# Optimization experiments

Hardware: AMD Instinct MI355X
Metric: run time of the kernel (lower is better)

## Reference

```python
import jax, jax.numpy as jnp
import numpy as np


def setup_inputs() -> dict:
    key = jax.random.key(0)
    k1, k2 = jax.random.split(key)
    n, B = 64, 256
    return {
        "out_matrix": jax.random.normal(k1, (n, n, B), dtype=jnp.float32),
        "label_matrix": jax.random.normal(k2, (n, n, B), dtype=jnp.float32),
        "margin": jnp.ones((), dtype=jnp.float32),
        "sample_num": 64,
    }


def reference(out_matrix, label_matrix, margin, sample_num):
    # out_matrix, label_matrix: [n, n, B]; sample_num == n (rows fully used).
    out = jnp.transpose(out_matrix, (2, 0, 1))   # [B, n, n]
    lab = jnp.transpose(label_matrix, (2, 0, 1))  # [B, n, n]
    # Per batch slice, per row r: pairwise diffs d[j,k] = out[r,j]-out[r,k]
    d = out[..., :, None] - out[..., None, :]     # [B, n, n, n]
    l = lab[..., :, None] - lab[..., None, :]     # [B, n, n, n]
    # Hinge: relu(margin - d*l), summed over everything (diagonal contributes margin,
    # matching the original which includes j==k terms).
    loss = jnp.sum(jax.nn.relu(margin - d * l))
    # flat_accuracy per batch slice: argmax over dim 1 of the [n,n] slice,
    # i.e. axis=2 of the [B,n,n] layout (torch argmax(preds,1) on squeezed slice).
    correction_num = jnp.sum(jnp.argmax(out, axis=2) == jnp.argmax(lab, axis=2))
    return loss, correction_num
```

## Files before the change

### kernel.cpp

```cpp
#include <hip/hip_runtime.h>
#include <math.h>


constexpr int N = 64;
constexpr int B = 256;
constexpr int BCHUNK = 64;
constexpr int NJG = 16;
constexpr int JI = 4;
constexpr int THREADS = BCHUNK * NJG;
constexpr int NBLK = N * (B / BCHUNK);

__global__ __launch_bounds__(THREADS)
void pm_hinge_partial(const float* __restrict__ outm,
                      const float* __restrict__ labm,
                      const float* __restrict__ margin,
                      float* __restrict__ ws)
{
    __shared__ float o_s[N * BCHUNK];
    __shared__ float l_s[N * BCHUNK];
    __shared__ float wsum[NJG];

    const int r   = blockIdx.x;
    const int b0  = blockIdx.y * BCHUNK;
    const int t   = threadIdx.x;
    const int blk = blockIdx.y * N + r;

    const float* src_o = outm + (size_t)r * (N * B) + b0;
    const float* src_l = labm + (size_t)r * (N * B) + b0;
#pragma unroll
    for (int f = t; f < (N * BCHUNK) / 4; f += THREADS) {
        const int j  = f >> 4;
        const int b4 = (f & 15) * 4;
        *(float4*)(&o_s[j * BCHUNK + b4]) = *(const float4*)(src_o + j * B + b4);
        *(float4*)(&l_s[j * BCHUNK + b4]) = *(const float4*)(src_l + j * B + b4);
    }
    __syncthreads();

    const float m  = margin[0];
    const int   b  = t & 63;
    const int   jg = t >> 6;

    float oj[JI], lj[JI];
#pragma unroll
    for (int i = 0; i < JI; ++i) {
        oj[i] = o_s[(jg + NJG * i) * BCHUNK + b];
        lj[i] = l_s[(jg + NJG * i) * BCHUNK + b];
    }

    float acc = 0.0f;

#define TERM(i) acc += fmaxf(fmaf(-(oj[i] - ok), lj[i] - lk, m), 0.0f)

#pragma unroll 4
    for (int k = jg + 1; k <= jg + 16; ++k) {
        const float ok = o_s[k * BCHUNK + b], lk = l_s[k * BCHUNK + b];
        TERM(0);
    }
#pragma unroll 4
    for (int k = jg + 17; k <= jg + 32; ++k) {
        const float ok = o_s[k * BCHUNK + b], lk = l_s[k * BCHUNK + b];
        TERM(0); TERM(1);
    }
#pragma unroll 4
    for (int k = jg + 33; k <= jg + 48; ++k) {
        const float ok = o_s[k * BCHUNK + b], lk = l_s[k * BCHUNK + b];
        TERM(0); TERM(1); TERM(2);
    }
#pragma unroll 2
    for (int k = jg + 49; k < N; ++k) {
        const float ok = o_s[k * BCHUNK + b], lk = l_s[k * BCHUNK + b];
        TERM(0); TERM(1); TERM(2); TERM(3);
    }
#undef TERM

    float cnt = 0.0f;
    if (t < 64) {
        const int bb = t;
        float bo = o_s[bb]; int io = 0;
        float bl = l_s[bb]; int il = 0;
#pragma unroll 4
        for (int j = 1; j < N; ++j) {
            const float vo = o_s[j * BCHUNK + bb];
            if (vo > bo) { bo = vo; io = j; }
            const float vl = l_s[j * BCHUNK + bb];
            if (vl > bl) { bl = vl; il = j; }
        }
        const unsigned long long mask = __ballot(io == il);
        cnt = (float)__popcll(mask);
    }

#pragma unroll
    for (int off = 32; off > 0; off >>= 1)
        acc += __shfl_down(acc, off, 64);
    if (b == 0) wsum[jg] = acc;
    __syncthreads();
    if (t == 0) {
        float s = 0.0f;
#pragma unroll
        for (int w = 0; w < NJG; ++w) s += wsum[w];
        ws[blk] = s;
        ws[NBLK + blk] = cnt;
    }
}

__global__ __launch_bounds__(64)
void pm_hinge_reduce(const float* __restrict__ ws,
                     const float* __restrict__ margin,
                     float* __restrict__ dout)
{
    const int t = threadIdx.x;
    float s = 0.0f, c = 0.0f;
#pragma unroll
    for (int i = 0; i < NBLK / 64; ++i) {
        s += ws[t + 64 * i];
        c += ws[NBLK + t + 64 * i];
    }
#pragma unroll
    for (int off = 32; off > 0; off >>= 1) {
        s += __shfl_down(s, off, 64);
        c += __shfl_down(c, off, 64);
    }
    if (t == 0) {
        const float m = margin[0];
        dout[0] = 2.0f * s + (float)(N * (size_t)N * B) * fmaxf(m, 0.0f);
        dout[1] = c;
    }
}

extern "C" void kernel_launch(void* const* d_in, const int* in_sizes, int n_in,
                              void* d_out, int out_size, void* d_ws, size_t ws_size,
                              hipStream_t stream) {
    const float* outm   = (const float*)d_in[0];
    const float* labm   = (const float*)d_in[1];
    const float* margin = (const float*)d_in[2];
    float* out = (float*)d_out;
    float* ws  = (float*)d_ws;

    pm_hinge_partial<<<dim3(N, B / BCHUNK), THREADS, 0, stream>>>(outm, labm, margin, ws);
    pm_hinge_reduce<<<1, 64, 0, stream>>>(ws, margin, out);
}
```

Baseline: 68.66 us.

## Interleave out/label in shared memory and widen per-thread j register blocking

Shared memory now stores out and label values interleaved as float2, so each k step needs a single 64-bit LDS load instead of two 32-bit loads. The thread count per block is halved (8 j-groups of 8 rows each), so every loaded k value is reused across up to 8 register-held j values and LDS traffic per pair term drops. The triangular loop is fully unrolled in 8-wide bands. In exchange each block has fewer waves to hide latency, register pressure rises, and the fully unrolled body grows larger.

```diff
diff --git a/kernel.cpp b/kernel.cpp
--- a/kernel.cpp
+++ b/kernel.cpp
@@ -5,8 +5,8 @@
 constexpr int N = 64;
 constexpr int B = 256;
 constexpr int BCHUNK = 64;
-constexpr int NJG = 16;
-constexpr int JI = 4;
+constexpr int NJG = 8;
+constexpr int JG = 8;
 constexpr int THREADS = BCHUNK * NJG;
 constexpr int NBLK = N * (B / BCHUNK);
 
@@ -16,8 +16,7 @@
                       const float* __restrict__ margin,
                       float* __restrict__ ws)
 {
-    __shared__ float o_s[N * BCHUNK];
-    __shared__ float l_s[N * BCHUNK];
+    __shared__ float2 ol[N * BCHUNK];
     __shared__ float wsum[NJG];
 
     const int r   = blockIdx.x;
@@ -31,59 +30,56 @@
     for (int f = t; f < (N * BCHUNK) / 4; f += THREADS) {
         const int j  = f >> 4;
         const int b4 = (f & 15) * 4;
-        *(float4*)(&o_s[j * BCHUNK + b4]) = *(const float4*)(src_o + j * B + b4);
-        *(float4*)(&l_s[j * BCHUNK + b4]) = *(const float4*)(src_l + j * B + b4);
+        const float4 vo = *(const float4*)(src_o + j * B + b4);
+        const float4 vl = *(const float4*)(src_l + j * B + b4);
+        float4 p0 = make_float4(vo.x, vl.x, vo.y, vl.y);
+        float4 p1 = make_float4(vo.z, vl.z, vo.w, vl.w);
+        *(float4*)(&ol[j * BCHUNK + b4])     = p0;
+        *(float4*)(&ol[j * BCHUNK + b4 + 2]) = p1;
     }
     __syncthreads();
 
-    const float m  = margin[0];
+    const float mg = margin[0];
     const int   b  = t & 63;
     const int   jg = t >> 6;
 
-    float oj[JI], lj[JI];
+    float oj[JG], lj[JG];
 #pragma unroll
-    for (int i = 0; i < JI; ++i) {
-        oj[i] = o_s[(jg + NJG * i) * BCHUNK + b];
-        lj[i] = l_s[(jg + NJG * i) * BCHUNK + b];
+    for (int i = 0; i < JG; ++i) {
+        const float2 v = ol[(jg + NJG * i) * BCHUNK + b];
+        oj[i] = v.x; lj[i] = v.y;
     }
 
     float acc = 0.0f;
-
-#define TERM(i) acc += fmaxf(fmaf(-(oj[i] - ok), lj[i] - lk, m), 0.0f)
-
-#pragma unroll 4
-    for (int k = jg + 1; k <= jg + 16; ++k) {
-        const float ok = o_s[k * BCHUNK + b], lk = l_s[k * BCHUNK + b];
-        TERM(0);
+#pragma unroll
+    for (int m = 0; m < 7; ++m) {
+#pragma unroll
+        for (int kk = 1; kk <= 8; ++kk) {
+            const int k = jg + 8 * m + kk;
+            const float2 olk = ol[k * BCHUNK + b];
+#pragma unroll
+            for (int i = 0; i <= m; ++i)
+                acc += fmaxf(fmaf(-(oj[i] - olk.x), lj[i] - olk.y, mg), 0.0f);
+        }
     }
-#pragma unroll 4
-    for (int k = jg + 17; k <= jg + 32; ++k) {
-        const float ok = o_s[k * BCHUNK + b], lk = l_s[k * BCHUNK + b];
-        TERM(0); TERM(1);
+    for (int k = jg + 57; k < N; ++k) {
+        const float2 olk = ol[k * BCHUNK + b];
+#pragma unroll
+        for (int i = 0; i < JG; ++i)
+            acc += fmaxf(fmaf(-(oj[i] - olk.x), lj[i] - olk.y, mg), 0.0f);
     }
-#pragma unroll 4
-    for (int k = jg + 33; k <= jg + 48; ++k) {
-        const float ok = o_s[k * BCHUNK + b], lk = l_s[k * BCHUNK + b];
-        TERM(0); TERM(1); TERM(2);
-    }
-#pragma unroll 2
-    for (int k = jg + 49; k < N; ++k) {
-        const float ok = o_s[k * BCHUNK + b], lk = l_s[k * BCHUNK + b];
-        TERM(0); TERM(1); TERM(2); TERM(3);
-    }
-#undef TERM
 
     float cnt = 0.0f;
     if (t < 64) {
         const int bb = t;
-        float bo = o_s[bb]; int io = 0;
-        float bl = l_s[bb]; int il = 0;
+        float2 v0 = ol[bb];
+        float bo = v0.x; int io = 0;
+        float bl = v0.y; int il = 0;
 #pragma unroll 4
         for (int j = 1; j < N; ++j) {
-            const float vo = o_s[j * BCHUNK + bb];
-            if (vo > bo) { bo = vo; io = j; }
-            const float vl = l_s[j * BCHUNK + bb];
-            if (vl > bl) { bl = vl; il = j; }
+            const float2 v = ol[j * BCHUNK + bb];
+            if (v.x > bo) { bo = v.x; io = j; }
+            if (v.y > bl) { bl = v.y; il = j; }
         }
         const unsigned long long mask = __ballot(io == il);
         cnt = (float)__popcll(mask);
```

Result: no change. 69.49 us (+1.2%).
